# Performance work log

Hardware: AMD Instinct MI355X
Metric: run time of the kernel (lower is better)

The kernel has to match this reference:

```python
import jax, jax.numpy as jnp
import numpy as np


def setup_inputs() -> dict:
    key = jax.random.key(0)
    N, D = 262144, 64
    x = jax.random.normal(key, (N, D), dtype=jnp.float32)
    return {"x": x, "n_clusters": 256, "n_iter": 10}


def reference(x, n_clusters, n_iter):
    # Faithful KMeans.fit: centroids init = first K rows; each iter assigns
    # points to nearest centroid (squared L2) then recomputes centroids via
    # per-cluster mean (bincount scatter-reduce in the original).
    N, D = x.shape
    K = n_clusters
    c0 = x[:K, :]
    x_sq = jnp.sum(x * x, axis=1)  # [N], reused every iteration

    def step(carry, _):
        c, _ = carry
        # squared distances ||x - c||^2 expanded: same math as ((x_i - c_j)**2).sum(-1)
        c_sq = jnp.sum(c * c, axis=1)                      # [K]
        d = x_sq[:, None] - 2.0 * (x @ c.T) + c_sq[None, :]  # [N, K]
        cl = jnp.argmin(d, axis=1)                          # [N] labels vs OLD centroids
        ones = jnp.ones((N,), dtype=x.dtype)
        Ncl = jax.ops.segment_sum(ones, cl, num_segments=K)  # bincount(cl)
        sums = jax.ops.segment_sum(x, cl, num_segments=K)    # per-dim weighted bincount
        new_c = sums / Ncl[:, None]
        return (new_c, cl), None

    cl0 = jnp.zeros((N,), dtype=jnp.int32)
    (c, cl), _ = jax.lax.scan(step, (c0, cl0), None, length=n_iter)
    return c, cl
```

## Files before the change

kernel.cpp:

```cpp
#include <hip/hip_runtime.h>
#include <hip/hip_bf16.h>

#define KC 256
#define DIM 64
#define NITER 10
#define SB 64
#define CPAD 66

typedef __attribute__((ext_vector_type(16))) float f32x16;
typedef __attribute__((ext_vector_type(4)))  float f32x4;
typedef __attribute__((ext_vector_type(8)))  short bf16x8;

__device__ __forceinline__ float np_pairwise_sq64(const float* a) {
    float r[8];
#pragma unroll
    for (int j = 0; j < 8; ++j) r[j] = __fmul_rn(a[j], a[j]);
#pragma unroll
    for (int i = 8; i < 64; i += 8)
#pragma unroll
        for (int j = 0; j < 8; ++j)
            r[j] = __fadd_rn(r[j], __fmul_rn(a[i + j], a[i + j]));
    float t01 = __fadd_rn(r[0], r[1]), t23 = __fadd_rn(r[2], r[3]);
    float t45 = __fadd_rn(r[4], r[5]), t67 = __fadd_rn(r[6], r[7]);
    return __fadd_rn(__fadd_rn(t01, t23), __fadd_rn(t45, t67));
}

__device__ __forceinline__ unsigned short f2bf(float f) {
    __hip_bfloat16 h = __float2bfloat16(f);
    return *reinterpret_cast<unsigned short*>(&h);
}

__global__ void init_k(const float* __restrict__ x, float* __restrict__ c) {
    const int idx = blockIdx.x * 256 + threadIdx.x;
    if (idx < KC * DIM) c[idx] = x[idx];
}

__global__ __launch_bounds__(256) void xinit_k(
    const float* __restrict__ x, unsigned short* __restrict__ xbf,
    float* __restrict__ xsq_g, int n)
{
    const int i = blockIdx.x * 256 + threadIdx.x;
    if (i >= n) return;
    float xr[DIM];
    const float4* xv = reinterpret_cast<const float4*>(x + (size_t)i * DIM);
    unsigned short* xb = xbf + (size_t)i * DIM;
#pragma unroll
    for (int j = 0; j < DIM / 4; ++j) {
        float4 v = xv[j];
        xr[4 * j + 0] = v.x; xr[4 * j + 1] = v.y;
        xr[4 * j + 2] = v.z; xr[4 * j + 3] = v.w;
        xb[4 * j + 0] = f2bf(v.x); xb[4 * j + 1] = f2bf(v.y);
        xb[4 * j + 2] = f2bf(v.z); xb[4 * j + 3] = f2bf(v.w);
    }
    xsq_g[i] = np_pairwise_sq64(xr);
}

__global__ __launch_bounds__(256) void csqg_k(
    const float* __restrict__ c, float* __restrict__ csq_g, int* __restrict__ nan_g)
{
    const int k = threadIdx.x;
    if (k == 0) *nan_g = 0x7fffffff;
    __syncthreads();
    float cr[DIM];
    const float4* cp = reinterpret_cast<const float4*>(c + k * DIM);
#pragma unroll
    for (int j = 0; j < DIM / 4; ++j) {
        float4 v = cp[j];
        cr[4 * j + 0] = v.x; cr[4 * j + 1] = v.y;
        cr[4 * j + 2] = v.z; cr[4 * j + 3] = v.w;
    }
    const float s = np_pairwise_sq64(cr);
    csq_g[k] = s;
    if (s != s) atomicMin(nan_g, k);
}

__global__ __launch_bounds__(256) void csqg2_k(
    const float* __restrict__ c, float* __restrict__ csq_g, int* __restrict__ nan_g,
    unsigned short* __restrict__ cbf, float* __restrict__ csqmax_g)
{
    __shared__ float smax[256];
    const int k = threadIdx.x;
    if (k == 0) *nan_g = 0x7fffffff;
    __syncthreads();
    float cr[DIM];
    const float4* cp = reinterpret_cast<const float4*>(c + k * DIM);
    unsigned short* cb = cbf + (size_t)k * DIM;
#pragma unroll
    for (int j = 0; j < DIM / 4; ++j) {
        float4 v = cp[j];
        cr[4 * j + 0] = v.x; cr[4 * j + 1] = v.y;
        cr[4 * j + 2] = v.z; cr[4 * j + 3] = v.w;
        cb[4 * j + 0] = f2bf(v.x); cb[4 * j + 1] = f2bf(v.y);
        cb[4 * j + 2] = f2bf(v.z); cb[4 * j + 3] = f2bf(v.w);
    }
    const float s = np_pairwise_sq64(cr);
    csq_g[k] = s;
    if (s != s) atomicMin(nan_g, k);
    smax[k] = (s == s) ? s : 0.0f;
    __syncthreads();
    for (int d = 128; d >= 1; d >>= 1) {
        if (k < d) smax[k] = fmaxf(smax[k], smax[k + d]);
        __syncthreads();
    }
    if (k == 0) *csqmax_g = smax[0];
}

__global__ __launch_bounds__(256) void assign_mfma_k(
    const float* __restrict__ x, const unsigned short* __restrict__ xbf,
    const float* __restrict__ xsq_g, const float* __restrict__ c,
    const unsigned short* __restrict__ cbf, const float* __restrict__ csq_g,
    const float* __restrict__ csqmax_g, const int* __restrict__ nan_g,
    float* __restrict__ labels, int* __restrict__ hist, int n)
{
    __shared__ unsigned short c_lds[128 * CPAD];
    __shared__ float csq_lds[KC];
    __shared__ int u_shm[1024];
    __shared__ int ccnt[256];

    short* cand = reinterpret_cast<short*>(u_shm);
    const int t = threadIdx.x;
    const int p0 = blockIdx.x * 256;

    csq_lds[t] = csq_g[t];
    ccnt[t] = 0;
    const float csqmax = *csqmax_g;
    const int firstNan = *nan_g;

    const int w = t >> 6, l = t & 63;
    const int grp = l >> 4, lr = l & 15;

    float rm[4][4];
#pragma unroll
    for (int q = 0; q < 4; ++q)
#pragma unroll
        for (int p = 0; p < 4; ++p) rm[q][p] = 3.4e38f;

#pragma unroll
    for (int h = 0; h < 2; ++h) {
        __syncthreads();
        for (int idx = t; idx < 128 * 8; idx += 256) {
            const int row = idx >> 3, ch = idx & 7;
            *reinterpret_cast<bf16x8*>(&c_lds[row * CPAD + ch * 8]) =
                *reinterpret_cast<const bf16x8*>(cbf + (size_t)(h * 128 + row) * DIM + ch * 8);
        }
        __syncthreads();
#pragma unroll
        for (int q = 0; q < 4; ++q) {
            const int pbase = p0 + w * 64 + q * 16;
            const unsigned short* xb = xbf + (size_t)(pbase + lr) * DIM;
            const bf16x8 a0 = *reinterpret_cast<const bf16x8*>(xb + grp * 8);
            const bf16x8 a1 = *reinterpret_cast<const bf16x8*>(xb + 32 + grp * 8);
            const int prow = pbase + grp * 4;
            const float xs0 = xsq_g[prow + 0], xs1 = xsq_g[prow + 1];
            const float xs2 = xsq_g[prow + 2], xs3 = xsq_g[prow + 3];
#pragma unroll
            for (int ct = 0; ct < 8; ++ct) {
                const unsigned short* cb = &c_lds[(ct * 16 + lr) * CPAD];
                const bf16x8 b0 = *reinterpret_cast<const bf16x8*>(cb + grp * 8);
                const bf16x8 b1 = *reinterpret_cast<const bf16x8*>(cb + 32 + grp * 8);
                f32x4 acc = {0.f, 0.f, 0.f, 0.f};
                acc = __builtin_amdgcn_mfma_f32_16x16x32_bf16(a0, b0, acc, 0, 0, 0);
                acc = __builtin_amdgcn_mfma_f32_16x16x32_bf16(a1, b1, acc, 0, 0, 0);
                const float cs = csq_lds[h * 128 + ct * 16 + lr];
                rm[q][0] = fminf(rm[q][0], __fadd_rn(fmaf(-2.0f, acc[0], xs0), cs));
                rm[q][1] = fminf(rm[q][1], __fadd_rn(fmaf(-2.0f, acc[1], xs1), cs));
                rm[q][2] = fminf(rm[q][2], __fadd_rn(fmaf(-2.0f, acc[2], xs2), cs));
                rm[q][3] = fminf(rm[q][3], __fadd_rn(fmaf(-2.0f, acc[3], xs3), cs));
            }
        }
    }

#pragma unroll
    for (int q = 0; q < 4; ++q) {
#pragma unroll
        for (int m = 1; m < 16; m <<= 1) {
            rm[q][0] = fminf(rm[q][0], __shfl_xor(rm[q][0], m, 64));
            rm[q][1] = fminf(rm[q][1], __shfl_xor(rm[q][1], m, 64));
            rm[q][2] = fminf(rm[q][2], __shfl_xor(rm[q][2], m, 64));
            rm[q][3] = fminf(rm[q][3], __shfl_xor(rm[q][3], m, 64));
        }
    }

#pragma unroll
    for (int h = 0; h < 2; ++h) {
        __syncthreads();
        for (int idx = t; idx < 128 * 8; idx += 256) {
            const int row = idx >> 3, ch = idx & 7;
            *reinterpret_cast<bf16x8*>(&c_lds[row * CPAD + ch * 8]) =
                *reinterpret_cast<const bf16x8*>(cbf + (size_t)(h * 128 + row) * DIM + ch * 8);
        }
        __syncthreads();
#pragma unroll
        for (int q = 0; q < 4; ++q) {
            const int pbase = p0 + w * 64 + q * 16;
            const unsigned short* xb = xbf + (size_t)(pbase + lr) * DIM;
            const bf16x8 a0 = *reinterpret_cast<const bf16x8*>(xb + grp * 8);
            const bf16x8 a1 = *reinterpret_cast<const bf16x8*>(xb + 32 + grp * 8);
            const int prow = pbase + grp * 4;
            const float xs0 = xsq_g[prow + 0], xs1 = xsq_g[prow + 1];
            const float xs2 = xsq_g[prow + 2], xs3 = xsq_g[prow + 3];
            const float th0 = rm[q][0] + 2.0f * (0.00399f * sqrtf(xs0 * csqmax) + 0.02f);
            const float th1 = rm[q][1] + 2.0f * (0.00399f * sqrtf(xs1 * csqmax) + 0.02f);
            const float th2 = rm[q][2] + 2.0f * (0.00399f * sqrtf(xs2 * csqmax) + 0.02f);
            const float th3 = rm[q][3] + 2.0f * (0.00399f * sqrtf(xs3 * csqmax) + 0.02f);
            const int pidx0 = w * 64 + q * 16 + grp * 4;
#pragma unroll
            for (int ct = 0; ct < 8; ++ct) {
                const unsigned short* cb = &c_lds[(ct * 16 + lr) * CPAD];
                const bf16x8 b0 = *reinterpret_cast<const bf16x8*>(cb + grp * 8);
                const bf16x8 b1 = *reinterpret_cast<const bf16x8*>(cb + 32 + grp * 8);
                f32x4 acc = {0.f, 0.f, 0.f, 0.f};
                acc = __builtin_amdgcn_mfma_f32_16x16x32_bf16(a0, b0, acc, 0, 0, 0);
                acc = __builtin_amdgcn_mfma_f32_16x16x32_bf16(a1, b1, acc, 0, 0, 0);
                const int kcol = h * 128 + ct * 16 + lr;
                const float cs = csq_lds[kcol];
                const float d0 = __fadd_rn(fmaf(-2.0f, acc[0], xs0), cs);
                const float d1 = __fadd_rn(fmaf(-2.0f, acc[1], xs1), cs);
                const float d2 = __fadd_rn(fmaf(-2.0f, acc[2], xs2), cs);
                const float d3 = __fadd_rn(fmaf(-2.0f, acc[3], xs3), cs);
                if (d0 <= th0) { int s = atomicAdd(&ccnt[pidx0 + 0], 1); if (s < 8) cand[(pidx0 + 0) * 8 + s] = (short)kcol; }
                if (d1 <= th1) { int s = atomicAdd(&ccnt[pidx0 + 1], 1); if (s < 8) cand[(pidx0 + 1) * 8 + s] = (short)kcol; }
                if (d2 <= th2) { int s = atomicAdd(&ccnt[pidx0 + 2], 1); if (s < 8) cand[(pidx0 + 2) * 8 + s] = (short)kcol; }
                if (d3 <= th3) { int s = atomicAdd(&ccnt[pidx0 + 3], 1); if (s < 8) cand[(pidx0 + 3) * 8 + s] = (short)kcol; }
            }
        }
    }
    __syncthreads();

    const int i = p0 + t;
    const bool valid = (i < n);
    int lbl = 0;
    if (valid) {
        const int nc = ccnt[t];
        if (firstNan != 0x7fffffff) {
            lbl = firstNan;
        } else if (nc == 1) {
            lbl = (int)cand[t * 8];
        } else {
            const float xsqv = xsq_g[i];
            const float4* xrow = reinterpret_cast<const float4*>(x + (size_t)i * DIM);
            float bd = 3.4e38f;
            int bk = 0;
            const bool fullscan = (nc == 0) || (nc > 8);
            const int lim = fullscan ? KC : nc;
            for (int s = 0; s < lim; ++s) {
                const int k = fullscan ? s : (int)cand[t * 8 + s];
                const float4* crow = reinterpret_cast<const float4*>(c + (size_t)k * DIM);
                float acc = 0.0f;
#pragma unroll
                for (int db = 0; db < 16; ++db) {
                    const float4 a = xrow[db], b = crow[db];
                    acc = fmaf(a.x, b.x, acc); acc = fmaf(a.y, b.y, acc);
                    acc = fmaf(a.z, b.z, acc); acc = fmaf(a.w, b.w, acc);
                }
                const float dd = __fadd_rn(fmaf(-2.0f, acc, xsqv), csq_lds[k]);
                if (dd < bd) { bd = dd; bk = k; }
                else if (dd == bd && k < bk) bk = k;
            }
            lbl = bk;
        }
        labels[i] = (float)lbl;
    }
    __syncthreads();

    int* whist = u_shm;
    for (int j = t; j < 4 * KC; j += 256) whist[j] = 0;
    __syncthreads();
    const int lane = t & 63, wv = t >> 6;
    unsigned long long same = __ballot(valid);
#pragma unroll
    for (int bit = 0; bit < 8; ++bit) {
        unsigned long long bb = __ballot((lbl >> bit) & 1);
        same &= ((lbl >> bit) & 1) ? bb : ~bb;
    }
    if (valid && lane == __builtin_ctzll(same))
        whist[wv * KC + lbl] = (int)__popcll(same);
    __syncthreads();
    if (t < KC)
        hist[(size_t)blockIdx.x * KC + t] =
            whist[t] + whist[KC + t] + whist[2 * KC + t] + whist[3 * KC + t];
}

__global__ __launch_bounds__(256) void assign_hist_k(
    const float* __restrict__ x, const float* __restrict__ c,
    const float* __restrict__ csq_g, const int* __restrict__ nan_g,
    float* __restrict__ labels, int* __restrict__ hist, int n)
{
    __shared__ int whist[4 * KC];
    const int t = threadIdx.x;
    for (int j = t; j < 4 * KC; j += 256) whist[j] = 0;

    const int i = blockIdx.x * 256 + t;
    const bool valid = (i < n);

    float xr[DIM];
    const float4* xv = reinterpret_cast<const float4*>(x + (size_t)(valid ? i : 0) * DIM);
#pragma unroll
    for (int j = 0; j < DIM / 4; ++j) {
        float4 v = xv[j];
        xr[4 * j + 0] = v.x; xr[4 * j + 1] = v.y;
        xr[4 * j + 2] = v.z; xr[4 * j + 3] = v.w;
    }
    const float xsq = np_pairwise_sq64(xr);
    const int firstNan = *nan_g;

    float best = __int_as_float(0x7f800000);
    int bk = 0;

#pragma unroll 1
    for (int k = 0; k < KC; ++k) {
        f32x16 h0, h1, h2, h3;
        float cs;
        const float* rp = c + (size_t)k * DIM;
        asm volatile("s_load_dwordx16 %0, %1, 0x0"  : "=s"(h0) : "s"(rp));
        asm volatile("s_load_dwordx16 %0, %1, 0x40" : "=s"(h1) : "s"(rp));
        asm volatile("s_load_dwordx16 %0, %1, 0x80" : "=s"(h2) : "s"(rp));
        asm volatile("s_load_dwordx16 %0, %1, 0xc0" : "=s"(h3) : "s"(rp));
        asm volatile("s_load_dword %0, %1, 0x0"     : "=s"(cs) : "s"(csq_g + k));
        asm volatile("s_waitcnt lgkmcnt(0)"
                     : "+s"(h0), "+s"(h1), "+s"(h2), "+s"(h3), "+s"(cs));
        __builtin_amdgcn_sched_barrier(0);

        float acc = 0.0f;
#pragma unroll
        for (int d = 0; d < 16; ++d) acc = fmaf(xr[d],      h0[d], acc);
#pragma unroll
        for (int d = 0; d < 16; ++d) acc = fmaf(xr[16 + d], h1[d], acc);
#pragma unroll
        for (int d = 0; d < 16; ++d) acc = fmaf(xr[32 + d], h2[d], acc);
#pragma unroll
        for (int d = 0; d < 16; ++d) acc = fmaf(xr[48 + d], h3[d], acc);

        const float dist = __fadd_rn(fmaf(-2.0f, acc, xsq), cs);
        if (dist < best) { best = dist; bk = k; }
    }

    int lbl = 0;
    if (valid) {
        lbl = (firstNan != 0x7fffffff) ? firstNan : bk;
        labels[i] = (float)lbl;
    }

    __syncthreads();
    const int lane = t & 63, w = t >> 6;
    unsigned long long same = __ballot(valid);
#pragma unroll
    for (int bit = 0; bit < 8; ++bit) {
        unsigned long long bb = __ballot((lbl >> bit) & 1);
        same &= ((lbl >> bit) & 1) ? bb : ~bb;
    }
    if (valid && lane == __builtin_ctzll(same))
        whist[w * KC + lbl] = (int)__popcll(same);
    __syncthreads();
    if (t < KC)
        hist[(size_t)blockIdx.x * KC + t] =
            whist[t] + whist[KC + t] + whist[2 * KC + t] + whist[3 * KC + t];
}

__global__ __launch_bounds__(256) void scan1_k(
    int* __restrict__ hist, int nb, int* __restrict__ cnt)
{
    __shared__ int sbuf[256];
    const int k = blockIdx.x;
    const int t = threadIdx.x;
    const int epb = (nb + 255) / 256;
    const int b0 = t * epb;

    int s = 0;
    for (int u = 0; u < epb; ++u) {
        const int b = b0 + u;
        if (b < nb) s += hist[(size_t)b * KC + k];
    }
    sbuf[t] = s;
    __syncthreads();
    int incl = s;
#pragma unroll
    for (int d = 1; d < 256; d <<= 1) {
        const int v = (t >= d) ? sbuf[t - d] : 0;
        __syncthreads();
        incl += v;
        sbuf[t] = incl;
        __syncthreads();
    }
    int run = incl - s;
    for (int u = 0; u < epb; ++u) {
        const int b = b0 + u;
        if (b < nb) {
            const int v = hist[(size_t)b * KC + k];
            hist[(size_t)b * KC + k] = run;
            run += v;
        }
    }
    if (t == 255) cnt[k] = incl;
}

__global__ __launch_bounds__(256) void scan2_k(
    const int* __restrict__ cnt, int* __restrict__ base)
{
    __shared__ int sbuf[256];
    const int t = threadIdx.x;
    const int padded = (cnt[t] + 63) & ~63;
    sbuf[t] = padded;
    __syncthreads();
    int incl = padded;
#pragma unroll
    for (int d = 1; d < 256; d <<= 1) {
        const int v = (t >= d) ? sbuf[t - d] : 0;
        __syncthreads();
        incl += v;
        sbuf[t] = incl;
        __syncthreads();
    }
    base[t] = incl - padded;
}

__global__ __launch_bounds__(256) void scatter_k(
    const float* __restrict__ labels, const int* __restrict__ hist,
    const int* __restrict__ base, int* __restrict__ order, int n)
{
    __shared__ int whist[4 * KC];
    const int t = threadIdx.x;
    for (int j = t; j < 4 * KC; j += 256) whist[j] = 0;
    __syncthreads();

    const int i = blockIdx.x * 256 + t;
    const bool valid = (i < n);
    const int lbl = valid ? (int)labels[i] : 0;
    const int lane = t & 63, w = t >> 6;

    unsigned long long same = __ballot(valid);
#pragma unroll
    for (int bit = 0; bit < 8; ++bit) {
        unsigned long long bb = __ballot((lbl >> bit) & 1);
        same &= ((lbl >> bit) & 1) ? bb : ~bb;
    }
    const unsigned long long below = (1ull << lane) - 1ull;
    const int rank_wave = (int)__popcll(same & below);
    if (valid && lane == __builtin_ctzll(same))
        whist[w * KC + lbl] = (int)__popcll(same);
    __syncthreads();

    if (valid) {
        int off = rank_wave;
        for (int ww = 0; ww < w; ++ww) off += whist[ww * KC + lbl];
        const int pos = base[lbl] + hist[(size_t)blockIdx.x * KC + lbl] + off;
        order[pos] = i;
    }
}

__global__ __launch_bounds__(256) void permute_k(
    const float* __restrict__ x, const int* __restrict__ order,
    float* __restrict__ xs)
{
    const int r = blockIdx.x * 4 + (threadIdx.x >> 6);
    const int d = threadIdx.x & 63;
    const int idx = order[r];
    float v = 0.0f;
    if (idx >= 0) v = x[(size_t)idx * DIM + d];
    xs[(size_t)r * DIM + d] = v;
}

#define LB(dst, off)                                                        \
    _Pragma("unroll")                                                       \
    for (int u = 0; u < SB; ++u) dst[u] = s[(size_t)((off) + u) * DIM];
#define AB(src)                                                             \
    _Pragma("unroll")                                                       \
    for (int u = 0; u < SB; ++u) acc = __fadd_rn(acc, src[u]);

__global__ __launch_bounds__(64) void sum2_k(
    const float* __restrict__ xs, const int* __restrict__ base,
    const int* __restrict__ cnt, float* __restrict__ c)
{
    const int k = blockIdx.x;
    const int lane = threadIdx.x;
    const int b0 = base[k];
    const int ct = cnt[k];
    const int ctp = (ct + 63) & ~63;
    const float* s = xs + (size_t)b0 * DIM + lane;

    float va[SB], vb[SB], vc[SB];
    float acc = 0.0f;

    if (ctp >= 2 * SB) {
        LB(va, 0)
        LB(vb, SB)
        int j = 0;
        for (; j + 5 * SB <= ctp; j += 3 * SB) {
            LB(vc, j + 2 * SB)
            AB(va)
            LB(va, j + 3 * SB)
            AB(vb)
            LB(vb, j + 4 * SB)
            AB(vc)
        }
        const int rem = ctp - j;
        AB(va)
        AB(vb)
        if (rem >= 3 * SB) {
            LB(vc, j + 2 * SB)
            AB(vc)
        }
        if (rem >= 4 * SB) {
            LB(va, j + 3 * SB)
            AB(va)
        }
    } else if (ctp == SB) {
        LB(va, 0)
        AB(va)
    }
    c[k * DIM + lane] = __fdiv_rn(acc, (float)ct);
}

__global__ __launch_bounds__(64) void gather_k(
    const float* __restrict__ x, const int* __restrict__ order,
    const int* __restrict__ base, const int* __restrict__ cnt,
    float* __restrict__ c)
{
    const int k = blockIdx.x;
    const int lane = threadIdx.x;
    const int b0 = base[k];
    const int ct = cnt[k];
    float acc = 0.0f;
    int j = 0;
    for (; j + 32 <= ct; j += 32) {
        float v[32];
#pragma unroll
        for (int u = 0; u < 32; ++u)
            v[u] = x[(size_t)order[b0 + j + u] * DIM + lane];
#pragma unroll
        for (int u = 0; u < 32; ++u) acc = __fadd_rn(acc, v[u]);
    }
    for (; j < ct; ++j)
        acc = __fadd_rn(acc, x[(size_t)order[b0 + j] * DIM + lane]);
    c[k * DIM + lane] = __fdiv_rn(acc, (float)ct);
}

extern "C" void kernel_launch(void* const* d_in, const int* in_sizes, int n_in,
                              void* d_out, int out_size, void* d_ws, size_t ws_size,
                              hipStream_t stream)
{
    const float* x = (const float*)d_in[0];
    const int n = in_sizes[0] / DIM;

    float* out_c = (float*)d_out;
    float* out_labels = out_c + KC * DIM;

    const int nb = (n + 255) / 256;
    const int nstride = n + KC * 64;

    size_t off = 0;
    auto alloc = [&](size_t bytes) -> size_t {
        size_t o = off; off = (off + bytes + 255) & ~(size_t)255; return o;
    };
    char*  w        = (char*)d_ws;
    float* csq_g    = (float*)(w + alloc(KC * sizeof(float)));
    int*   nan_g    = (int*)(w + alloc(256));
    float* csqmax_g = (float*)(w + alloc(256));
    unsigned short* cbf_g = (unsigned short*)(w + alloc(KC * DIM * sizeof(unsigned short)));
    int*   hist  = (int*)(w + alloc((size_t)nb * KC * sizeof(int)));
    int*   base  = (int*)(w + alloc(KC * sizeof(int)));
    int*   cnt   = (int*)(w + alloc(KC * sizeof(int)));
    int*   order = (int*)(w + alloc((size_t)nstride * sizeof(int)));
    const size_t med_need = off;
    float* xs    = (float*)(w + alloc((size_t)nstride * DIM * sizeof(float)));
    const size_t big_need = off;
    unsigned short* xbf = (unsigned short*)(w + alloc((size_t)n * DIM * sizeof(unsigned short)));
    float* xsq_g = (float*)(w + alloc((size_t)n * sizeof(float)));
    const size_t huge_need = off;

    const bool med  = (ws_size >= med_need);
    const bool big  = (ws_size >= big_need);
    const bool huge = (ws_size >= huge_need);

    init_k<<<(KC * DIM + 255) / 256, 256, 0, stream>>>(x, out_c);
    if (huge)
        xinit_k<<<nb, 256, 0, stream>>>(x, xbf, xsq_g, n);

    for (int it = 0; it < NITER; ++it) {
        if (huge) {
            csqg2_k<<<1, 256, 0, stream>>>(out_c, csq_g, nan_g, cbf_g, csqmax_g);
            assign_mfma_k<<<nb, 256, 0, stream>>>(x, xbf, xsq_g, out_c, cbf_g,
                                                  csq_g, csqmax_g, nan_g,
                                                  out_labels, hist, n);
        } else {
            csqg_k<<<1, 256, 0, stream>>>(out_c, csq_g, nan_g);
            assign_hist_k<<<nb, 256, 0, stream>>>(x, out_c, csq_g, nan_g,
                                                  out_labels, hist, n);
        }
        if (med) {
            scan1_k<<<KC, 256, 0, stream>>>(hist, nb, cnt);
            scan2_k<<<1, 256, 0, stream>>>(cnt, base);
            if (big) {
                (void)hipMemsetAsync(order, 0xFF, (size_t)nstride * sizeof(int), stream);
                scatter_k<<<nb, 256, 0, stream>>>(out_labels, hist, base, order, n);
                permute_k<<<nstride / 4, 256, 0, stream>>>(x, order, xs);
                sum2_k<<<KC, 64, 0, stream>>>(xs, base, cnt, out_c);
            } else {
                scatter_k<<<nb, 256, 0, stream>>>(out_labels, hist, base, order, n);
                gather_k<<<KC, 64, 0, stream>>>(x, order, base, cnt, out_c);
            }
        }
    }
}
```

Measured before the change: 1.639 ms.

## Permute points into dimension-major buffer and sum clusters with vector loads

The per-iteration permute now goes through a shared-memory tile and writes sorted points in a dimension-major layout (one row per feature of length nstride). The centroid-sum kernel then lets each lane walk contiguous memory for its own dimension using float4 loads, with triple-buffered register blocks instead of scalar strided loads. The goal is higher bandwidth and fewer load instructions in the reduction. The cost is an extra shared-memory transpose in the permute, and loads in the sum that are strided by nstride across lanes, which may coalesce worse.

Result: no change. 1.660 ms (+1.3%).

```diff
diff --git a/kernel.cpp b/kernel.cpp
--- a/kernel.cpp
+++ b/kernel.cpp
@@ -4,7 +4,6 @@
 #define KC 256
 #define DIM 64
 #define NITER 10
-#define SB 64
 #define CPAD 66
 
 typedef __attribute__((ext_vector_type(16))) float f32x16;
@@ -448,65 +447,79 @@
     }
 }
 
-__global__ __launch_bounds__(256) void permute_k(
+__global__ __launch_bounds__(256) void transpose_k(
     const float* __restrict__ x, const int* __restrict__ order,
-    float* __restrict__ xs)
-{
-    const int r = blockIdx.x * 4 + (threadIdx.x >> 6);
-    const int d = threadIdx.x & 63;
-    const int idx = order[r];
-    float v = 0.0f;
-    if (idx >= 0) v = x[(size_t)idx * DIM + d];
-    xs[(size_t)r * DIM + d] = v;
-}
-
-#define LB(dst, off)                                                        \
-    _Pragma("unroll")                                                       \
-    for (int u = 0; u < SB; ++u) dst[u] = s[(size_t)((off) + u) * DIM];
-#define AB(src)                                                             \
-    _Pragma("unroll")                                                       \
-    for (int u = 0; u < SB; ++u) acc = __fadd_rn(acc, src[u]);
-
-__global__ __launch_bounds__(64) void sum2_k(
-    const float* __restrict__ xs, const int* __restrict__ base,
-    const int* __restrict__ cnt, float* __restrict__ c)
+    float* __restrict__ buf, int nstride)
+{
+    __shared__ float tile[64][65];
+    __shared__ int idxs[64];
+    const int t = threadIdx.x;
+    const int p0 = blockIdx.x * 64;
+    if (t < 64) idxs[t] = order[p0 + t];
+    __syncthreads();
+    const int w = t >> 6, lane = t & 63;
+#pragma unroll
+    for (int r = 0; r < 16; ++r) {
+        const int row = w * 16 + r;
+        const int idx = idxs[row];
+        tile[row][lane] = (idx >= 0) ? x[(size_t)idx * DIM + lane] : 0.0f;
+    }
+    __syncthreads();
+#pragma unroll
+    for (int r = 0; r < 16; ++r) {
+        const int d = w * 16 + r;
+        buf[(size_t)d * nstride + p0 + lane] = tile[lane][d];
+    }
+}
+
+#define LBN(P, off) {                                                       \
+    const f32x4* p4_ = reinterpret_cast<const f32x4*>(s + (off));           \
+    P##0 = p4_[0]; P##1 = p4_[1]; P##2 = p4_[2]; P##3 = p4_[3];             \
+    P##4 = p4_[4]; P##5 = p4_[5]; P##6 = p4_[6]; P##7 = p4_[7]; }
+#define AB1(V) acc = __fadd_rn(acc, V.x); acc = __fadd_rn(acc, V.y);        \
+               acc = __fadd_rn(acc, V.z); acc = __fadd_rn(acc, V.w);
+#define ABN(P) AB1(P##0) AB1(P##1) AB1(P##2) AB1(P##3)                      \
+               AB1(P##4) AB1(P##5) AB1(P##6) AB1(P##7)
+
+__global__ __launch_bounds__(64) void sum3_k(
+    const float* __restrict__ buf, const int* __restrict__ base,
+    const int* __restrict__ cnt, float* __restrict__ c, int nstride)
 {
     const int k = blockIdx.x;
     const int lane = threadIdx.x;
     const int b0 = base[k];
     const int ct = cnt[k];
     const int ctp = (ct + 63) & ~63;
-    const float* s = xs + (size_t)b0 * DIM + lane;
-
-    float va[SB], vb[SB], vc[SB];
+    const float* s = buf + (size_t)lane * nstride + b0;
+
+    f32x4 A0, A1, A2, A3, A4, A5, A6, A7;
+    f32x4 B0, B1, B2, B3, B4, B5, B6, B7;
+    f32x4 C0, C1, C2, C3, C4, C5, C6, C7;
     float acc = 0.0f;
 
-    if (ctp >= 2 * SB) {
-        LB(va, 0)
-        LB(vb, SB)
+    if (ctp >= 64) {
+        LBN(A, 0)
+        LBN(B, 32)
         int j = 0;
-        for (; j + 5 * SB <= ctp; j += 3 * SB) {
-            LB(vc, j + 2 * SB)
-            AB(va)
-            LB(va, j + 3 * SB)
-            AB(vb)
-            LB(vb, j + 4 * SB)
-            AB(vc)
+        for (; j + 160 <= ctp; j += 96) {
+            LBN(C, j + 64)
+            ABN(A)
+            LBN(A, j + 96)
+            ABN(B)
+            LBN(B, j + 128)
+            ABN(C)
         }
         const int rem = ctp - j;
-        AB(va)
-        AB(vb)
-        if (rem >= 3 * SB) {
-            LB(vc, j + 2 * SB)
-            AB(vc)
-        }
-        if (rem >= 4 * SB) {
-            LB(va, j + 3 * SB)
-            AB(va)
-        }
-    } else if (ctp == SB) {
-        LB(va, 0)
-        AB(va)
+        ABN(A)
+        ABN(B)
+        if (rem >= 96) {
+            LBN(C, j + 64)
+            ABN(C)
+        }
+        if (rem >= 128) {
+            LBN(A, j + 96)
+            ABN(A)
+        }
     }
     c[k * DIM + lane] = __fdiv_rn(acc, (float)ct);
 }
@@ -562,7 +575,7 @@
     int*   cnt   = (int*)(w + alloc(KC * sizeof(int)));
     int*   order = (int*)(w + alloc((size_t)nstride * sizeof(int)));
     const size_t med_need = off;
-    float* xs    = (float*)(w + alloc((size_t)nstride * DIM * sizeof(float)));
+    float* buf   = (float*)(w + alloc((size_t)nstride * DIM * sizeof(float)));
     const size_t big_need = off;
     unsigned short* xbf = (unsigned short*)(w + alloc((size_t)n * DIM * sizeof(unsigned short)));
     float* xsq_g = (float*)(w + alloc((size_t)n * sizeof(float)));
@@ -593,8 +606,8 @@
             if (big) {
                 (void)hipMemsetAsync(order, 0xFF, (size_t)nstride * sizeof(int), stream);
                 scatter_k<<<nb, 256, 0, stream>>>(out_labels, hist, base, order, n);
-                permute_k<<<nstride / 4, 256, 0, stream>>>(x, order, xs);
-                sum2_k<<<KC, 64, 0, stream>>>(xs, base, cnt, out_c);
+                transpose_k<<<nstride / 64, 256, 0, stream>>>(x, order, buf, nstride);
+                sum3_k<<<KC, 64, 0, stream>>>(buf, base, cnt, out_c, nstride);
             } else {
                 scatter_k<<<nb, 256, 0, stream>>>(out_labels, hist, base, order, n);
                 gather_k<<<KC, 64, 0, stream>>>(x, order, base, cnt, out_c);
```

## Replace per-cluster sum kernel with producer/consumer LDS double-buffered reduction

Applied to the files above, without the earlier changes.

The per-cluster centroid sum kernel now runs 512 threads per cluster. Seven producer waves stream 128-row tiles of the permuted points into double-buffered shared memory with vectorized loads, while one consumer wave accumulates sequentially in the same order to keep bitwise results. This aims to raise memory-level parallelism over the old single-wave register-pipelined loop. In exchange it adds a barrier per tile, and the serial accumulation in one wave may still bound the runtime.

After: 1.766 ms. +7.7%, slower.

```diff
diff --git a/kernel.cpp b/kernel.cpp
--- a/kernel.cpp
+++ b/kernel.cpp
@@ -4,7 +4,6 @@
 #define KC 256
 #define DIM 64
 #define NITER 10
-#define SB 64
 #define CPAD 66
 
 typedef __attribute__((ext_vector_type(16))) float f32x16;
@@ -460,55 +459,56 @@
     xs[(size_t)r * DIM + d] = v;
 }
 
-#define LB(dst, off)                                                        \
-    _Pragma("unroll")                                                       \
-    for (int u = 0; u < SB; ++u) dst[u] = s[(size_t)((off) + u) * DIM];
-#define AB(src)                                                             \
-    _Pragma("unroll")                                                       \
-    for (int u = 0; u < SB; ++u) acc = __fadd_rn(acc, src[u]);
-
-__global__ __launch_bounds__(64) void sum2_k(
+#define SUMBR 128
+
+__global__ __launch_bounds__(512) void sum4_k(
     const float* __restrict__ xs, const int* __restrict__ base,
     const int* __restrict__ cnt, float* __restrict__ c)
 {
+    __shared__ float sbuf[2][SUMBR * DIM];
+
     const int k = blockIdx.x;
-    const int lane = threadIdx.x;
+    const int t = threadIdx.x;
+    const int w = t >> 6;
+    const int lane = t & 63;
     const int b0 = base[k];
     const int ct = cnt[k];
     const int ctp = (ct + 63) & ~63;
-    const float* s = xs + (size_t)b0 * DIM + lane;
-
-    float va[SB], vb[SB], vc[SB];
+    const int nbt = (ctp + SUMBR - 1) / SUMBR;
+
+    const f32x4* src4 = reinterpret_cast<const f32x4*>(xs + (size_t)b0 * DIM);
+
+    if (w < 7 && nbt > 0) {
+        const int bs4 = ((ctp < SUMBR) ? ctp : SUMBR) * 16;
+        f32x4* dst4 = reinterpret_cast<f32x4*>(sbuf[0]);
+        for (int idx = t; idx < bs4; idx += 448)
+            dst4[idx] = src4[idx];
+    }
+    __syncthreads();
+
     float acc = 0.0f;
-
-    if (ctp >= 2 * SB) {
-        LB(va, 0)
-        LB(vb, SB)
-        int j = 0;
-        for (; j + 5 * SB <= ctp; j += 3 * SB) {
-            LB(vc, j + 2 * SB)
-            AB(va)
-            LB(va, j + 3 * SB)
-            AB(vb)
-            LB(vb, j + 4 * SB)
-            AB(vc)
-        }
-        const int rem = ctp - j;
-        AB(va)
-        AB(vb)
-        if (rem >= 3 * SB) {
-            LB(vc, j + 2 * SB)
-            AB(vc)
-        }
-        if (rem >= 4 * SB) {
-            LB(va, j + 3 * SB)
-            AB(va)
-        }
-    } else if (ctp == SB) {
-        LB(va, 0)
-        AB(va)
-    }
-    c[k * DIM + lane] = __fdiv_rn(acc, (float)ct);
+    for (int b = 0; b < nbt; ++b) {
+        if (w < 7) {
+            if (b + 1 < nbt) {
+                const int jb = (b + 1) * SUMBR;
+                const int rows = ((ctp - jb) < SUMBR) ? (ctp - jb) : SUMBR;
+                const int bs4 = rows * 16;
+                f32x4* dst4 = reinterpret_cast<f32x4*>(sbuf[(b + 1) & 1]);
+                for (int idx = t; idx < bs4; idx += 448)
+                    dst4[idx] = src4[(size_t)jb * 16 + idx];
+            }
+        } else {
+            const int jb = b * SUMBR;
+            const int rows = ((ctp - jb) < SUMBR) ? (ctp - jb) : SUMBR;
+            const float* sb = &sbuf[b & 1][lane];
+            for (int r = 0; r < rows; ++r)
+                acc = __fadd_rn(acc, sb[(size_t)r * DIM]);
+        }
+        __syncthreads();
+    }
+
+    if (w == 7)
+        c[k * DIM + lane] = __fdiv_rn(acc, (float)ct);
 }
 
 __global__ __launch_bounds__(64) void gather_k(
@@ -594,7 +594,7 @@
                 (void)hipMemsetAsync(order, 0xFF, (size_t)nstride * sizeof(int), stream);
                 scatter_k<<<nb, 256, 0, stream>>>(out_labels, hist, base, order, n);
                 permute_k<<<nstride / 4, 256, 0, stream>>>(x, order, xs);
-                sum2_k<<<KC, 64, 0, stream>>>(xs, base, cnt, out_c);
+                sum4_k<<<KC, 512, 0, stream>>>(xs, base, cnt, out_c);
             } else {
                 scatter_k<<<nb, 256, 0, stream>>>(out_labels, hist, base, order, n);
                 gather_k<<<KC, 64, 0, stream>>>(x, order, base, cnt, out_c);
```
